# Performance work log

Hardware: AMD Instinct MI355X
Metric: run time of the kernel (lower is better)

## Reference

```python
import jax, jax.numpy as jnp
import numpy as np
from jax import lax

PAD = 2          # shift_size // 2
CHUNKS = 5       # shift_size


def shift(x, H, W, D, axis):
    # x: (B, N, C) with N = H*W*D; axis in {2,3,4} of the (B,C,H,W,D) view
    B, N, C = x.shape
    xn = x.transpose(0, 2, 1).reshape(B, C, H, W, D)
    xn = jnp.pad(xn, ((0, 0), (0, 0), (PAD, PAD), (PAD, PAD), (PAD, PAD)))
    xs = jnp.split(xn, CHUNKS, axis=1)
    rolled = [jnp.roll(xc, s, axis) for xc, s in zip(xs, range(-PAD, PAD + 1))]
    xc = jnp.concatenate(rolled, axis=1)
    xc = xc[:, :, PAD:PAD + H, PAD:PAD + W, PAD:PAD + D]
    return xc.reshape(B, C, H * W * D).transpose(0, 2, 1)


def dwconv(x, k, b, H, W, D):
    # depthwise 3x3x3 conv; x: (B,N,C), k: (C,1,3,3,3), b: (C,)
    B, N, C = x.shape
    v = x.transpose(0, 2, 1).reshape(B, C, H, W, D)
    y = lax.conv_general_dilated(
        v, k, window_strides=(1, 1, 1), padding='SAME',
        feature_group_count=C,
        dimension_numbers=('NCDHW', 'OIDHW', 'NCDHW'))
    y = y + b[None, :, None, None, None]
    return y.reshape(B, C, N).transpose(0, 2, 1)


def setup_inputs() -> dict:
    key = jax.random.key(0)
    ks = jax.random.split(key, 12)
    B, H, W, D = 4, 32, 32, 32
    C = 160  # in = hidden = out
    N = H * W * D
    inp = {
        'x': jax.random.normal(ks[0], (B, N, C), jnp.float32),
        'H': H, 'W': W, 'D': D,
        'w1': jax.random.normal(ks[1], (C, C), jnp.float32) * 0.02,
        'b1': jnp.zeros((C,), jnp.float32),
        'dw1': jax.random.normal(ks[2], (C, 1, 3, 3, 3), jnp.float32) * 0.27,
        'bdw1': jnp.zeros((C,), jnp.float32),
        'w2': jax.random.normal(ks[3], (C, C), jnp.float32) * 0.02,
        'b2': jnp.zeros((C,), jnp.float32),
        'dw2': jax.random.normal(ks[4], (C, 1, 3, 3, 3), jnp.float32) * 0.27,
        'bdw2': jnp.zeros((C,), jnp.float32),
        'w3': jax.random.normal(ks[5], (C, C), jnp.float32) * 0.02,
        'b3': jnp.zeros((C,), jnp.float32),
    }
    return inp


def reference(x, H, W, D, w1, b1, dw1, bdw1, w2, b2, dw2, bdw2, w3, b3):
    x = shift(x, H, W, D, axis=2)
    x = x @ w1 + b1                       # fc1 (drop p=0)
    x = dwconv(x, dw1, bdw1, H, W, D)
    x = shift(x, H, W, D, axis=3)
    x = x @ w2 + b2                       # fc2
    x = dwconv(x, dw2, bdw2, H, W, D)
    x = shift(x, H, W, D, axis=4)
    x = x @ w3 + b3                       # fc3
    x = jax.nn.gelu(x, approximate=False) # nn.GELU default (exact erf)
    return x
```

## Files before the change

### kernel.cpp

```cpp
#include <hip/hip_runtime.h>

typedef __bf16 bf16x8 __attribute__((ext_vector_type(8)));
typedef float f32x4 __attribute__((ext_vector_type(4)));

__device__ inline unsigned short f2bf(float f) {
    unsigned x = __builtin_bit_cast(unsigned, f);
    x += 0x7fffu + ((x >> 16) & 1u);
    return (unsigned short)(x >> 16);
}
__device__ inline unsigned pack2bf(float lo, float hi) {
    return (unsigned)f2bf(lo) | ((unsigned)f2bf(hi) << 16);
}
__device__ inline void cvt8(uint4 u, float* o) {
    o[0] = __builtin_bit_cast(float, u.x << 16);
    o[1] = __builtin_bit_cast(float, u.x & 0xffff0000u);
    o[2] = __builtin_bit_cast(float, u.y << 16);
    o[3] = __builtin_bit_cast(float, u.y & 0xffff0000u);
    o[4] = __builtin_bit_cast(float, u.z << 16);
    o[5] = __builtin_bit_cast(float, u.z & 0xffff0000u);
    o[6] = __builtin_bit_cast(float, u.w << 16);
    o[7] = __builtin_bit_cast(float, u.w & 0xffff0000u);
}
__device__ inline float gelu_f(float v) {
    float x = fabsf(v) * 0.70710678118654752f;
    float td = __builtin_amdgcn_rcpf(1.0f + 0.3275911f * x);
    float p = ((((1.061405429f * td - 1.453152027f) * td + 1.421413741f) * td
                - 0.284496736f) * td + 0.254829592f) * td;
    float e = __expf(-x * x);
    float er = 1.0f - p * e;
    float s = v < 0.0f ? -er : er;
    return 0.5f * v * (1.0f + s);
}

__device__ inline void gload_lds16(const void* g, void* l) {
    typedef __attribute__((address_space(1))) const unsigned int gq;
    typedef __attribute__((address_space(3))) unsigned int sq;
    __builtin_amdgcn_global_load_lds((gq*)g, (sq*)l, 16, 0, 0);
}

#define WPAD 168
#define WELEMS (160 * WPAD)
#define WCHUNKS (WELEMS * 2 / 16)

__global__ __launch_bounds__(256) void prep_w3(const float* __restrict__ W1,
                                               const float* __restrict__ W2,
                                               const float* __restrict__ W3,
                                               unsigned short* __restrict__ dst) {
    int e = blockIdx.x * 256 + threadIdx.x;
    if (e >= 3 * WELEMS) return;
    int m = e / WELEMS;
    int r = e - m * WELEMS;
    int co = r / WPAD, ci = r - co * WPAD;
    const float* W = (m == 0) ? W1 : (m == 1) ? W2 : W3;
    dst[e] = (ci < 160) ? f2bf(W[ci * 160 + co]) : (unsigned short)0;
}

template <int AXIS, bool FP32IN>
__device__ inline void load_a_raw(const void* __restrict__ Xv, int row, uint4* u,
                                  float4* f, int kq) {
    const int n = row & 32767;
    const int coord = (AXIS == 0) ? (n >> 10) : (AXIS == 1) ? ((n >> 5) & 31) : (n & 31);
    const int stride = (AXIS == 0) ? 1024 : (AXIS == 1) ? 32 : 1;
#pragma unroll
    for (int g = 0; g < 5; g++) {
        int s = 2 - g;
        bool ok = (unsigned)(coord + s) < 32u;
        int srow = ok ? row + s * stride : row;
        size_t off = (size_t)srow * 160 + g * 32 + kq * 8;
        if (FP32IN) {
            const float* p = (const float*)Xv + off;
            float4 r0 = ((const float4*)p)[0];
            float4 r1 = ((const float4*)p)[1];
            if (!ok) { r0 = make_float4(0, 0, 0, 0); r1 = make_float4(0, 0, 0, 0); }
            f[g * 2] = r0; f[g * 2 + 1] = r1;
        } else {
            uint4 v = *(const uint4*)((const unsigned short*)Xv + off);
            if (!ok) v = make_uint4(0, 0, 0, 0);
            u[g] = v;
        }
    }
}

template <bool FP32IN>
__device__ inline void pack_a(const uint4* u, const float4* f, uint4* a) {
#pragma unroll
    for (int g = 0; g < 5; g++) {
        if (FP32IN) {
            float4 r0 = f[g * 2], r1 = f[g * 2 + 1];
            a[g] = make_uint4(pack2bf(r0.x, r0.y), pack2bf(r0.z, r0.w),
                              pack2bf(r1.x, r1.y), pack2bf(r1.z, r1.w));
        } else {
            a[g] = u[g];
        }
    }
}

__device__ inline void tile_compute_both(const unsigned short* __restrict__ lw,
                                         const uint4* a0, const uint4* a1,
                                         f32x4* acc0, f32x4* acc1, int mr, int kq) {
#pragma unroll
    for (int g = 0; g < 5; g++) {
        bf16x8 x0 = __builtin_bit_cast(bf16x8, a0[g]);
        bf16x8 x1 = __builtin_bit_cast(bf16x8, a1[g]);
        const unsigned short* bp = lw + mr * WPAD + g * 32 + kq * 8;
#pragma unroll
        for (int nt = 0; nt < 10; nt++) {
            bf16x8 wf = __builtin_bit_cast(bf16x8, *(const uint4*)(bp + nt * 16 * WPAD));
            acc0[nt] = __builtin_amdgcn_mfma_f32_16x16x32_bf16(wf, x0, acc0[nt], 0, 0, 0);
            acc1[nt] = __builtin_amdgcn_mfma_f32_16x16x32_bf16(wf, x1, acc1[nt], 0, 0, 0);
        }
    }
}

__device__ inline void store_bf16_staged(unsigned short* __restrict__ stg,
                                         const f32x4* acc, const float* __restrict__ Bs,
                                         unsigned short* __restrict__ Yv, int rowbase,
                                         int lane, int wv, int mr, int kq) {
    unsigned short* sw = stg + wv * (16 * 168);
#pragma unroll
    for (int nt = 0; nt < 10; nt++) {
        float4 bb = *(const float4*)(Bs + nt * 16 + kq * 4);
        uint2 pk;
        pk.x = pack2bf(acc[nt][0] + bb.x, acc[nt][1] + bb.y);
        pk.y = pack2bf(acc[nt][2] + bb.z, acc[nt][3] + bb.w);
        *(uint2*)(sw + mr * 168 + nt * 16 + kq * 4) = pk;
    }
#pragma unroll
    for (int p = 0; p < 5; p++) {
        int idx = p * 512 + lane * 8;
        int row = idx / 160;
        int col = idx - row * 160;
        uint4 v = *(const uint4*)(sw + row * 168 + col);
        *(uint4*)(Yv + (size_t)rowbase * 160 + idx) = v;
    }
}

__device__ inline void store_f32_direct(const f32x4* acc, const float* __restrict__ Bs,
                                        float* __restrict__ Yv, int rowbase,
                                        int mr, int kq) {
    float* rp = Yv + (size_t)(rowbase + mr) * 160;
#pragma unroll
    for (int nt = 0; nt < 10; nt++) {
        float4 bb = *(const float4*)(Bs + nt * 16 + kq * 4);
        float4 v;
        v.x = gelu_f(acc[nt][0] + bb.x);
        v.y = gelu_f(acc[nt][1] + bb.y);
        v.z = gelu_f(acc[nt][2] + bb.z);
        v.w = gelu_f(acc[nt][3] + bb.w);
        *(float4*)(rp + nt * 16 + kq * 4) = v;
    }
}

template <int AXIS, bool GELU, bool FP32IN, bool F32OUT>
__global__ __launch_bounds__(256, 2) void gemm_shift(
    const void* __restrict__ Xv, const unsigned short* __restrict__ Wt,
    const float* __restrict__ Bs, void* __restrict__ Yv) {
    __shared__ unsigned short lw[WELEMS];
    __shared__ unsigned short stg[F32OUT ? 1 : 4 * 16 * 168];
    const int t = threadIdx.x;
    const int lane = t & 63, wv = t >> 6, mr = lane & 15, kq = lane >> 4;
    const int rbase = blockIdx.x * 256;

    for (int i = t; i < WCHUNKS; i += 256)
        gload_lds16((const char*)Wt + i * 16, (char*)lw + i * 16);

    uint4 u0[5], u1[5];
    float4 f0[10], f1[10];
    load_a_raw<AXIS, FP32IN>(Xv, rbase + wv * 16 + mr, u0, f0, kq);
    load_a_raw<AXIS, FP32IN>(Xv, rbase + 64 + wv * 16 + mr, u1, f1, kq);

    __syncthreads();

    uint4 a0[5], a1[5];
    pack_a<FP32IN>(u0, f0, a0);
    pack_a<FP32IN>(u1, f1, a1);

    load_a_raw<AXIS, FP32IN>(Xv, rbase + 128 + wv * 16 + mr, u0, f0, kq);
    load_a_raw<AXIS, FP32IN>(Xv, rbase + 192 + wv * 16 + mr, u1, f1, kq);

    f32x4 acc0[10] = {};
    f32x4 acc1[10] = {};
    tile_compute_both(lw, a0, a1, acc0, acc1, mr, kq);
    if (F32OUT) {
        store_f32_direct(acc0, Bs, (float*)Yv, rbase + wv * 16, mr, kq);
        store_f32_direct(acc1, Bs, (float*)Yv, rbase + 64 + wv * 16, mr, kq);
    } else {
        store_bf16_staged(stg, acc0, Bs, (unsigned short*)Yv, rbase + wv * 16, lane, wv, mr, kq);
        store_bf16_staged(stg, acc1, Bs, (unsigned short*)Yv, rbase + 64 + wv * 16, lane, wv, mr, kq);
    }

    pack_a<FP32IN>(u0, f0, a0);
    pack_a<FP32IN>(u1, f1, a1);
#pragma unroll
    for (int nt = 0; nt < 10; nt++) { acc0[nt] = f32x4{0, 0, 0, 0}; acc1[nt] = f32x4{0, 0, 0, 0}; }
    tile_compute_both(lw, a0, a1, acc0, acc1, mr, kq);
    if (F32OUT) {
        store_f32_direct(acc0, Bs, (float*)Yv, rbase + 128 + wv * 16, mr, kq);
        store_f32_direct(acc1, Bs, (float*)Yv, rbase + 192 + wv * 16, mr, kq);
    } else {
        store_bf16_staged(stg, acc0, Bs, (unsigned short*)Yv, rbase + 128 + wv * 16, lane, wv, mr, kq);
        store_bf16_staged(stg, acc1, Bs, (unsigned short*)Yv, rbase + 192 + wv * 16, lane, wv, mr, kq);
    }
}

__global__ __launch_bounds__(256) void dwconv3(
    const unsigned short* __restrict__ X, const float* __restrict__ Kw,
    const float* __restrict__ Bs, unsigned short* __restrict__ Y) {
    __shared__ float wl[20 * 220];
    const int t = threadIdx.x;
    for (int e = t; e < 160 * 27; e += 256) {
        int c = e / 27, tap = e % 27;
        wl[(c >> 3) * 220 + tap * 8 + (c & 7)] = Kw[e];
    }
    __syncthreads();

    int bid = blockIdx.x;
    int swz = (bid & 7) * 320 + (bid >> 3);
    int idx = swz * 256 + t;

    int cc = idx % 20;
    int r = idx / 20;
    int dq = r & 7;  r >>= 3;
    int w = r & 31;  r >>= 5;
    int h = r & 31;
    int b = r >> 5;
    int d0 = dq << 2;

    float acc[4][8];
    {
        float bv[8];
        *(float4*)&bv[0] = ((const float4*)(Bs + cc * 8))[0];
        *(float4*)&bv[4] = ((const float4*)(Bs + cc * 8))[1];
#pragma unroll
        for (int od = 0; od < 4; od++)
#pragma unroll
            for (int j = 0; j < 8; j++) acc[od][j] = bv[j];
    }
    const float* wbase = &wl[cc * 220];
#pragma unroll
    for (int dh = -1; dh <= 1; dh++) {
        int hh = h + dh;
        if ((unsigned)hh >= 32u) continue;
#pragma unroll
        for (int dwi = -1; dwi <= 1; dwi++) {
            int ww = w + dwi;
            if ((unsigned)ww >= 32u) continue;
            const unsigned short* base =
                X + (size_t)(b * 32768 + hh * 1024 + ww * 32) * 160 + cc * 8;
            int tap0 = (dh + 1) * 9 + (dwi + 1) * 3;
            float wv_[24];
#pragma unroll
            for (int q2 = 0; q2 < 6; q2++)
                ((float4*)wv_)[q2] = *(const float4*)(wbase + tap0 * 8 + q2 * 4);
            uint4 ub[6];
#pragma unroll
            for (int dd = 0; dd < 6; dd++) {
                int d = d0 - 1 + dd;
                ub[dd] = ((unsigned)d < 32u) ? *(const uint4*)(base + d * 160)
                                             : make_uint4(0, 0, 0, 0);
            }
            float vb[6][8];
#pragma unroll
            for (int dd = 0; dd < 6; dd++) cvt8(ub[dd], vb[dd]);
#pragma unroll
            for (int od = 0; od < 4; od++)
#pragma unroll
                for (int dd = 0; dd < 3; dd++)
#pragma unroll
                    for (int j = 0; j < 8; j++)
                        acc[od][j] += vb[od + dd][j] * wv_[dd * 8 + j];
        }
    }
#pragma unroll
    for (int od = 0; od < 4; od++) {
        unsigned short tmp[8];
#pragma unroll
        for (int j = 0; j < 8; j++) tmp[j] = f2bf(acc[od][j]);
        *(uint4*)(Y + (size_t)(b * 32768 + h * 1024 + w * 32 + d0 + od) * 160 + cc * 8) =
            *(uint4*)tmp;
    }
}

extern "C" void kernel_launch(void* const* d_in, const int* in_sizes, int n_in,
                              void* d_out, int out_size, void* d_ws, size_t ws_size,
                              hipStream_t stream) {
    const void*  x    = d_in[0];
    const float* w1   = (const float*)d_in[4];
    const float* b1   = (const float*)d_in[5];
    const float* dw1  = (const float*)d_in[6];
    const float* bdw1 = (const float*)d_in[7];
    const float* w2   = (const float*)d_in[8];
    const float* b2   = (const float*)d_in[9];
    const float* dw2  = (const float*)d_in[10];
    const float* bdw2 = (const float*)d_in[11];
    const float* w3   = (const float*)d_in[12];
    const float* b3   = (const float*)d_in[13];

    unsigned short* wbf = (unsigned short*)d_ws;

    const size_t BUF_BYTES = (size_t)4 * 32768 * 160 * 2;
    const size_t OFF_A = 2u << 20;
    const size_t OFF_B = OFF_A + BUF_BYTES;
    unsigned short* bufA;
    unsigned short* bufB;
    if (ws_size >= OFF_B + BUF_BYTES) {
        bufA = (unsigned short*)((char*)d_ws + OFF_A);
        bufB = (unsigned short*)((char*)d_ws + OFF_B);
    } else {
        bufA = (unsigned short*)d_out;
        bufB = (unsigned short*)d_in[0];
    }

    prep_w3<<<315, 256, 0, stream>>>(w1, w2, w3, wbf);
    gemm_shift<0, false, true,  false><<<512, 256, 0, stream>>>(x,    wbf,              b1, bufA);
    dwconv3<<<2560, 256, 0, stream>>>(bufA, dw1, bdw1, bufB);
    gemm_shift<1, false, false, false><<<512, 256, 0, stream>>>(bufB, wbf + WELEMS,     b2, bufA);
    dwconv3<<<2560, 256, 0, stream>>>(bufA, dw2, bdw2, bufB);
    gemm_shift<2, true,  false, true ><<<512, 256, 0, stream>>>(bufB, wbf + 2 * WELEMS, b3, d_out);
}
```

Baseline: 303.5 us.

## Split GEMM blocks over output-channel halves and row blocks for more parallelism

Each GEMM block now computes 128 rows by 80 output channels instead of 256 rows by all 160 channels. The grid grows fourfold with a swizzled block index, and launch bounds allow four blocks per CU. Each block loads only half the weight matrix into LDS, and the staging buffer shrinks. This raises occupancy and the number of blocks, at the cost of loading and shift-gathering every input row twice, once per channel half.

```diff
diff --git a/kernel.cpp b/kernel.cpp
--- a/kernel.cpp
+++ b/kernel.cpp
@@ -40,7 +40,10 @@
 
 #define WPAD 168
 #define WELEMS (160 * WPAD)
-#define WCHUNKS (WELEMS * 2 / 16)
+#define WHALF_ROWS 80
+#define WHALF_ELEMS (WHALF_ROWS * WPAD)
+#define WHALF_CHUNKS (WHALF_ELEMS * 2 / 16)
+#define SPAD 88
 
 __global__ __launch_bounds__(256) void prep_w3(const float* __restrict__ W1,
                                                const float* __restrict__ W2,
@@ -95,16 +98,16 @@
     }
 }
 
-__device__ inline void tile_compute_both(const unsigned short* __restrict__ lw,
-                                         const uint4* a0, const uint4* a1,
-                                         f32x4* acc0, f32x4* acc1, int mr, int kq) {
+__device__ inline void tile_compute_both_h(const unsigned short* __restrict__ lw,
+                                           const uint4* a0, const uint4* a1,
+                                           f32x4* acc0, f32x4* acc1, int mr, int kq) {
 #pragma unroll
     for (int g = 0; g < 5; g++) {
         bf16x8 x0 = __builtin_bit_cast(bf16x8, a0[g]);
         bf16x8 x1 = __builtin_bit_cast(bf16x8, a1[g]);
         const unsigned short* bp = lw + mr * WPAD + g * 32 + kq * 8;
 #pragma unroll
-        for (int nt = 0; nt < 10; nt++) {
+        for (int nt = 0; nt < 5; nt++) {
             bf16x8 wf = __builtin_bit_cast(bf16x8, *(const uint4*)(bp + nt * 16 * WPAD));
             acc0[nt] = __builtin_amdgcn_mfma_f32_16x16x32_bf16(wf, x0, acc0[nt], 0, 0, 0);
             acc1[nt] = __builtin_amdgcn_mfma_f32_16x16x32_bf16(wf, x1, acc1[nt], 0, 0, 0);
@@ -112,36 +115,37 @@
     }
 }
 
-__device__ inline void store_bf16_staged(unsigned short* __restrict__ stg,
-                                         const f32x4* acc, const float* __restrict__ Bs,
-                                         unsigned short* __restrict__ Yv, int rowbase,
-                                         int lane, int wv, int mr, int kq) {
-    unsigned short* sw = stg + wv * (16 * 168);
-#pragma unroll
-    for (int nt = 0; nt < 10; nt++) {
-        float4 bb = *(const float4*)(Bs + nt * 16 + kq * 4);
+__device__ inline void store_bf16_staged_h(unsigned short* __restrict__ stg,
+                                           const f32x4* acc, const float* __restrict__ Bs,
+                                           unsigned short* __restrict__ Yv, int rowbase,
+                                           int co0, int lane, int wv, int mr, int kq) {
+    unsigned short* sw = stg + wv * (16 * SPAD);
+#pragma unroll
+    for (int nt = 0; nt < 5; nt++) {
+        float4 bb = *(const float4*)(Bs + co0 + nt * 16 + kq * 4);
         uint2 pk;
         pk.x = pack2bf(acc[nt][0] + bb.x, acc[nt][1] + bb.y);
         pk.y = pack2bf(acc[nt][2] + bb.z, acc[nt][3] + bb.w);
-        *(uint2*)(sw + mr * 168 + nt * 16 + kq * 4) = pk;
-    }
-#pragma unroll
-    for (int p = 0; p < 5; p++) {
+        *(uint2*)(sw + mr * SPAD + nt * 16 + kq * 4) = pk;
+    }
+#pragma unroll
+    for (int p = 0; p < 3; p++) {
         int idx = p * 512 + lane * 8;
-        int row = idx / 160;
-        int col = idx - row * 160;
-        uint4 v = *(const uint4*)(sw + row * 168 + col);
-        *(uint4*)(Yv + (size_t)rowbase * 160 + idx) = v;
-    }
-}
-
-__device__ inline void store_f32_direct(const f32x4* acc, const float* __restrict__ Bs,
-                                        float* __restrict__ Yv, int rowbase,
-                                        int mr, int kq) {
-    float* rp = Yv + (size_t)(rowbase + mr) * 160;
-#pragma unroll
-    for (int nt = 0; nt < 10; nt++) {
-        float4 bb = *(const float4*)(Bs + nt * 16 + kq * 4);
+        if (p == 2 && lane >= 32) break;
+        int row = idx / 80;
+        int col = idx - row * 80;
+        uint4 v = *(const uint4*)(sw + row * SPAD + col);
+        *(uint4*)(Yv + (size_t)(rowbase + row) * 160 + co0 + col) = v;
+    }
+}
+
+__device__ inline void store_f32_direct_h(const f32x4* acc, const float* __restrict__ Bs,
+                                          float* __restrict__ Yv, int rowbase,
+                                          int co0, int mr, int kq) {
+    float* rp = Yv + (size_t)(rowbase + mr) * 160 + co0;
+#pragma unroll
+    for (int nt = 0; nt < 5; nt++) {
+        float4 bb = *(const float4*)(Bs + co0 + nt * 16 + kq * 4);
         float4 v;
         v.x = gelu_f(acc[nt][0] + bb.x);
         v.y = gelu_f(acc[nt][1] + bb.y);
@@ -152,17 +156,24 @@
 }
 
 template <int AXIS, bool GELU, bool FP32IN, bool F32OUT>
-__global__ __launch_bounds__(256, 2) void gemm_shift(
+__global__ __launch_bounds__(256, 4) void gemm_shift(
     const void* __restrict__ Xv, const unsigned short* __restrict__ Wt,
     const float* __restrict__ Bs, void* __restrict__ Yv) {
-    __shared__ unsigned short lw[WELEMS];
-    __shared__ unsigned short stg[F32OUT ? 1 : 4 * 16 * 168];
+    __shared__ unsigned short lw[WHALF_ELEMS];
+    __shared__ unsigned short stg[F32OUT ? 1 : 4 * 16 * SPAD];
     const int t = threadIdx.x;
     const int lane = t & 63, wv = t >> 6, mr = lane & 15, kq = lane >> 4;
-    const int rbase = blockIdx.x * 256;
-
-    for (int i = t; i < WCHUNKS; i += 256)
-        gload_lds16((const char*)Wt + i * 16, (char*)lw + i * 16);
+
+    int bid = blockIdx.x;
+    int swz = (bid & 7) * 256 + (bid >> 3);
+    const int rowblk = swz >> 1;
+    const int cohalf = swz & 1;
+    const int rbase = rowblk * 128;
+    const int co0 = cohalf * 80;
+    const unsigned short* wth = Wt + cohalf * WHALF_ELEMS;
+
+    for (int i = t; i < WHALF_CHUNKS; i += 256)
+        gload_lds16((const char*)wth + i * 16, (char*)lw + i * 16);
 
     uint4 u0[5], u1[5];
     float4 f0[10], f1[10];
@@ -174,32 +185,18 @@
     uint4 a0[5], a1[5];
     pack_a<FP32IN>(u0, f0, a0);
     pack_a<FP32IN>(u1, f1, a1);
-
-    load_a_raw<AXIS, FP32IN>(Xv, rbase + 128 + wv * 16 + mr, u0, f0, kq);
-    load_a_raw<AXIS, FP32IN>(Xv, rbase + 192 + wv * 16 + mr, u1, f1, kq);
-
-    f32x4 acc0[10] = {};
-    f32x4 acc1[10] = {};
-    tile_compute_both(lw, a0, a1, acc0, acc1, mr, kq);
+    f32x4 acc0[5] = {};
+    f32x4 acc1[5] = {};
+    tile_compute_both_h(lw, a0, a1, acc0, acc1, mr, kq);
+
     if (F32OUT) {
-        store_f32_direct(acc0, Bs, (float*)Yv, rbase + wv * 16, mr, kq);
-        store_f32_direct(acc1, Bs, (float*)Yv, rbase + 64 + wv * 16, mr, kq);
+        store_f32_direct_h(acc0, Bs, (float*)Yv, rbase + wv * 16, co0, mr, kq);
+        store_f32_direct_h(acc1, Bs, (float*)Yv, rbase + 64 + wv * 16, co0, mr, kq);
     } else {
-        store_bf16_staged(stg, acc0, Bs, (unsigned short*)Yv, rbase + wv * 16, lane, wv, mr, kq);
-        store_bf16_staged(stg, acc1, Bs, (unsigned short*)Yv, rbase + 64 + wv * 16, lane, wv, mr, kq);
-    }
-
-    pack_a<FP32IN>(u0, f0, a0);
-    pack_a<FP32IN>(u1, f1, a1);
-#pragma unroll
-    for (int nt = 0; nt < 10; nt++) { acc0[nt] = f32x4{0, 0, 0, 0}; acc1[nt] = f32x4{0, 0, 0, 0}; }
-    tile_compute_both(lw, a0, a1, acc0, acc1, mr, kq);
-    if (F32OUT) {
-        store_f32_direct(acc0, Bs, (float*)Yv, rbase + 128 + wv * 16, mr, kq);
-        store_f32_direct(acc1, Bs, (float*)Yv, rbase + 192 + wv * 16, mr, kq);
-    } else {
-        store_bf16_staged(stg, acc0, Bs, (unsigned short*)Yv, rbase + 128 + wv * 16, lane, wv, mr, kq);
-        store_bf16_staged(stg, acc1, Bs, (unsigned short*)Yv, rbase + 192 + wv * 16, lane, wv, mr, kq);
+        store_bf16_staged_h(stg, acc0, Bs, (unsigned short*)Yv, rbase + wv * 16,
+                            co0, lane, wv, mr, kq);
+        store_bf16_staged_h(stg, acc1, Bs, (unsigned short*)Yv, rbase + 64 + wv * 16,
+                            co0, lane, wv, mr, kq);
     }
 }
 
@@ -312,9 +309,9 @@
     }
 
     prep_w3<<<315, 256, 0, stream>>>(w1, w2, w3, wbf);
-    gemm_shift<0, false, true,  false><<<512, 256, 0, stream>>>(x,    wbf,              b1, bufA);
+    gemm_shift<0, false, true,  false><<<2048, 256, 0, stream>>>(x,    wbf,              b1, bufA);
     dwconv3<<<2560, 256, 0, stream>>>(bufA, dw1, bdw1, bufB);
-    gemm_shift<1, false, false, false><<<512, 256, 0, stream>>>(bufB, wbf + WELEMS,     b2, bufA);
+    gemm_shift<1, false, false, false><<<2048, 256, 0, stream>>>(bufB, wbf + WELEMS,     b2, bufA);
     dwconv3<<<2560, 256, 0, stream>>>(bufA, dw2, bdw2, bufB);
-    gemm_shift<2, true,  false, true ><<<512, 256, 0, stream>>>(bufB, wbf + 2 * WELEMS, b3, d_out);
-}
+    gemm_shift<2, true,  false, true ><<<2048, 256, 0, stream>>>(bufB, wbf + 2 * WELEMS, b3, d_out);
+}
```

Result: no change. 298.0 us (-1.8%).
